# Optimization experiments

Hardware: AMD Instinct MI355X
Metric: run time of the kernel (lower is better)

Reference implementation:

```python
import jax, jax.numpy as jnp
import numpy as np

HIDDEN = 32  # hard-coded in EdgeModel's Sequential

def setup_inputs() -> dict:
    key = jax.random.key(0)
    ks = jax.random.split(key, 9)
    E, FN, FE, OUT = 200000, 512, 256, 128
    IN = FN + FN + FE  # 1280
    src = jax.random.normal(ks[0], (E, FN), dtype=jnp.float32)
    dest = jax.random.normal(ks[1], (E, FN), dtype=jnp.float32)
    edge_attr = jax.random.normal(ks[2], (E, FE), dtype=jnp.float32)
    u = jax.random.normal(ks[3], (64, 128), dtype=jnp.float32)
    batch = jax.random.randint(ks[4], (E,), 0, 64, dtype=jnp.int64)
    # Linear params, PyTorch default init scale ~ 1/sqrt(fan_in)
    s1 = 1.0 / np.sqrt(IN)
    s2 = 1.0 / np.sqrt(HIDDEN)
    W1 = jax.random.uniform(ks[5], (IN, HIDDEN), jnp.float32, -s1, s1)
    b1 = jax.random.uniform(ks[6], (HIDDEN,), jnp.float32, -s1, s1)
    W2 = jax.random.uniform(ks[7], (HIDDEN, OUT), jnp.float32, -s2, s2)
    b2 = jax.random.uniform(ks[8], (OUT,), jnp.float32, -s2, s2)
    return {"src": src, "dest": dest, "edge_attr": edge_attr, "u": u,
            "batch": batch, "W1": W1, "b1": b1, "W2": W2, "b2": b2}

def reference(src, dest, edge_attr, u, batch, W1, b1, W2, b2):
    # concat along feature dim, then Linear -> ELU -> Linear (u, batch unused)
    x = jnp.concatenate([src, dest, edge_attr], axis=1)  # [E, 2*FN+FE]
    h = jax.nn.elu(x @ W1 + b1)                           # [E, 32]
    return h @ W2 + b2                                    # [E, OUT]
```

## Files before the change

### kernel.cpp

```cpp
#include <hip/hip_runtime.h>
#include <hip/hip_bf16.h>

typedef __bf16 bf16x8 __attribute__((ext_vector_type(8)));
typedef unsigned short u16x8 __attribute__((ext_vector_type(8)));
typedef float f32x4 __attribute__((ext_vector_type(4)));
typedef unsigned int u32x4 __attribute__((ext_vector_type(4)));

using gptr_t = const __attribute__((address_space(1))) unsigned int*;
using lptr_t = __attribute__((address_space(3))) unsigned int*;

__global__ __launch_bounds__(256) void prep_w_kernel(
    const float* __restrict__ W1, const float* __restrict__ W2,
    unsigned short* __restrict__ wsB1, unsigned short* __restrict__ wsB2) {
  int tid = blockIdx.x * 256 + threadIdx.x;
  if (tid < 40960) {
    int j = tid & 7, l = (tid >> 3) & 63, nt = (tid >> 9) & 1, kt = tid >> 10;
    int k = kt * 32 + ((l >> 4) << 3) + j;
    int n = nt * 16 + (l & 15);
    __bf16 v = (__bf16)W1[k * 32 + n];
    wsB1[tid] = __builtin_bit_cast(unsigned short, v);
  } else if (tid < 45056) {
    int t = tid - 40960;
    int j = t & 7, l = (t >> 3) & 63, nt = t >> 9;
    int k = ((l >> 4) << 3) + j;
    int n = nt * 16 + (l & 15);
    __bf16 v = (__bf16)W2[k * 128 + n];
    wsB2[t] = __builtin_bit_cast(unsigned short, v);
  }
}

__device__ __forceinline__ u32x4 make_srd(const void* p, unsigned bytes) {
  u32x4 r;
  r[0] = (unsigned)(unsigned long long)p;
  r[1] = (unsigned)(((unsigned long long)p) >> 32);
  r[2] = bytes;
  r[3] = 0x00020000u;
  return r;
}

#define XLDS(SLOT, GP, FOFF)                                                   \
  do {                                                                         \
    __builtin_amdgcn_global_load_lds((gptr_t)(const void*)((GP) + (FOFF)),     \
                                     (lptr_t)(void*)(ringw + (SLOT) * 512),    \
                                     16, 0, 0);                                \
    __builtin_amdgcn_global_load_lds((gptr_t)(const void*)((GP) + (FOFF) + 4), \
                                     (lptr_t)(void*)(ringw + (SLOT) * 512 + 256), \
                                     16, 0, 0);                                \
  } while (0)
#define WLD(SLOT, SOFF)                                                    \
  asm volatile("buffer_load_dwordx4 %0, %2, %3, %4 offen offset:0"         \
               "\n\tbuffer_load_dwordx4 %1, %2, %3, %4 offen offset:1024"  \
               : "=&v"(pw[SLOT][0]), "=&v"(pw[SLOT][1])                    \
               : "v"(voffw), "s"(srdw), "s"((unsigned)(SOFF))              \
               : "memory")
#define VMW(N)                                                \
  do {                                                        \
    asm volatile("s_waitcnt vmcnt(" #N ")" ::: "memory");     \
    __builtin_amdgcn_sched_barrier(0);                        \
  } while (0)
#define CONS(SX, SW)                                                          \
  do {                                                                        \
    f32x4 lo, hi;                                                             \
    asm volatile("ds_read_b128 %0, %2\n\t"                                    \
                 "ds_read_b128 %1, %2 offset:1024\n\t"                        \
                 "s_waitcnt lgkmcnt(0)"                                       \
                 : "=&v"(lo), "=&v"(hi)                                       \
                 : "v"(ldsrd + (SX) * 2048u)                                  \
                 : "memory");                                                 \
    __builtin_amdgcn_sched_barrier(0);                                        \
    bf16x8 a;                                                                 \
    a[0] = (__bf16)lo[0]; a[1] = (__bf16)lo[1];                               \
    a[2] = (__bf16)lo[2]; a[3] = (__bf16)lo[3];                               \
    a[4] = (__bf16)hi[0]; a[5] = (__bf16)hi[1];                               \
    a[6] = (__bf16)hi[2]; a[7] = (__bf16)hi[3];                               \
    acc0 = __builtin_amdgcn_mfma_f32_16x16x32_bf16(                           \
        a, __builtin_bit_cast(bf16x8, pw[SW][0]), acc0, 0, 0, 0);             \
    acc1 = __builtin_amdgcn_mfma_f32_16x16x32_bf16(                           \
        a, __builtin_bit_cast(bf16x8, pw[SW][1]), acc1, 0, 0, 0);             \
  } while (0)

template <bool USE_WS>
__global__ __launch_bounds__(256, 3) void edge_mlp_kernel(
    const float* __restrict__ src, const float* __restrict__ dst,
    const float* __restrict__ ea, const float* __restrict__ W1,
    const float* __restrict__ b1, const float* __restrict__ W2,
    const float* __restrict__ b2, const unsigned short* __restrict__ wsB1,
    const unsigned short* __restrict__ wsB2, float* __restrict__ out, int nE) {
  __shared__ alignas(16) float ring_s[4][6][512];
  const int lane = threadIdx.x & 63;
  const int wave = threadIdx.x >> 6;
  const int l15 = lane & 15;
  const int lh = lane >> 4;
  const long strip = (long)blockIdx.x * 4 + wave;
  const long e0 = strip * 16;
  if (e0 >= nE) return;
  long row = e0 + l15;
  if (row >= nE) row = nE - 1;

  float* ringw = &ring_s[wave][0][0];
  const float bias0 = b1[l15];
  const float bias1 = b1[16 + l15];

  f32x4 acc0 = {0.f, 0.f, 0.f, 0.f};
  f32x4 acc1 = {0.f, 0.f, 0.f, 0.f};

  if constexpr (USE_WS) {
    const u32x4 srdw = make_srd(wsB1, 81920u);
    const unsigned voffw = (unsigned)lane * 16u;
    const float* psrc = src + row * 512 + lh * 8;
    const float* pdst = dst + row * 512 + lh * 8;
    const float* pea = ea + row * 256 + lh * 8;
    const unsigned ldsrd =
        (unsigned)(unsigned long long)(__attribute__((address_space(3))) void*)
            ringw + (unsigned)lane * 16u;

    u16x8 pw[4][2];

    XLDS(0, psrc, 0);    WLD(0, 0);
    XLDS(1, psrc, 32);   WLD(1, 2048);
    XLDS(2, psrc, 64);   WLD(2, 4096);
    XLDS(3, psrc, 96);   WLD(3, 6144);
    XLDS(4, psrc, 128);
    XLDS(5, psrc, 160);

    VMW(16); CONS(0, 0); XLDS(0, psrc, 192); WLD(0, 8192);
    VMW(16); CONS(1, 1); XLDS(1, psrc, 224); WLD(1, 10240);
    VMW(16); CONS(2, 2); XLDS(2, psrc, 256); WLD(2, 12288);
    VMW(16); CONS(3, 3); XLDS(3, psrc, 288); WLD(3, 14336);
    VMW(12); CONS(4, 0); XLDS(4, psrc, 320); WLD(0, 16384);
    VMW(12); CONS(5, 1); XLDS(5, psrc, 352); WLD(1, 18432);
    VMW(12); CONS(0, 2); XLDS(0, psrc, 384); WLD(2, 20480);
    VMW(12); CONS(1, 3); XLDS(1, psrc, 416); WLD(3, 22528);
    VMW(12); CONS(2, 0); XLDS(2, psrc, 448); WLD(0, 24576);
    VMW(12); CONS(3, 1); XLDS(3, psrc, 480); WLD(1, 26624);
    VMW(12); CONS(4, 2); XLDS(4, pdst, 0);   WLD(2, 28672);
    VMW(12); CONS(5, 3); XLDS(5, pdst, 32);  WLD(3, 30720);
    VMW(12); CONS(0, 0); XLDS(0, pdst, 64);  WLD(0, 32768);
    VMW(12); CONS(1, 1); XLDS(1, pdst, 96);  WLD(1, 34816);
    VMW(12); CONS(2, 2); XLDS(2, pdst, 128); WLD(2, 36864);
    VMW(12); CONS(3, 3); XLDS(3, pdst, 160); WLD(3, 38912);
    VMW(12); CONS(4, 0); XLDS(4, pdst, 192); WLD(0, 40960);
    VMW(12); CONS(5, 1); XLDS(5, pdst, 224); WLD(1, 43008);
    VMW(12); CONS(0, 2); XLDS(0, pdst, 256); WLD(2, 45056);
    VMW(12); CONS(1, 3); XLDS(1, pdst, 288); WLD(3, 47104);
    VMW(12); CONS(2, 0); XLDS(2, pdst, 320); WLD(0, 49152);
    VMW(12); CONS(3, 1); XLDS(3, pdst, 352); WLD(1, 51200);
    VMW(12); CONS(4, 2); XLDS(4, pdst, 384); WLD(2, 53248);
    VMW(12); CONS(5, 3); XLDS(5, pdst, 416); WLD(3, 55296);
    VMW(12); CONS(0, 0); XLDS(0, pdst, 448); WLD(0, 57344);
    VMW(12); CONS(1, 1); XLDS(1, pdst, 480); WLD(1, 59392);
    VMW(12); CONS(2, 2); XLDS(2, pea, 0);    WLD(2, 61440);
    VMW(12); CONS(3, 3); XLDS(3, pea, 32);   WLD(3, 63488);
    VMW(12); CONS(4, 0); XLDS(4, pea, 64);   WLD(0, 65536);
    VMW(12); CONS(5, 1); XLDS(5, pea, 96);   WLD(1, 67584);
    VMW(12); CONS(0, 2); XLDS(0, pea, 128);  WLD(2, 69632);
    VMW(12); CONS(1, 3); XLDS(1, pea, 160);  WLD(3, 71680);
    VMW(12); CONS(2, 0); XLDS(2, pea, 192);  WLD(0, 73728);
    VMW(12); CONS(3, 1); XLDS(3, pea, 224);  WLD(1, 75776);
    VMW(12); CONS(4, 2);                     WLD(2, 77824);
    VMW(10); CONS(5, 3);                     WLD(3, 79872);
    VMW(8);  CONS(0, 0);
    VMW(4);  CONS(1, 1);
    VMW(2);  CONS(2, 2);
    VMW(0);  CONS(3, 3);
  } else {
    for (int t = 0; t < 40; ++t) {
      const float* p = (t < 16) ? (src + row * 512 + t * 32 + lh * 8)
                     : (t < 32) ? (dst + row * 512 + (t - 16) * 32 + lh * 8)
                                : (ea + row * 256 + (t - 32) * 32 + lh * 8);
      f32x4 lo = *(const f32x4*)p;
      f32x4 hi = *(const f32x4*)(p + 4);
      bf16x8 a, bf0, bf1;
      a[0] = (__bf16)lo[0]; a[1] = (__bf16)lo[1];
      a[2] = (__bf16)lo[2]; a[3] = (__bf16)lo[3];
      a[4] = (__bf16)hi[0]; a[5] = (__bf16)hi[1];
      a[6] = (__bf16)hi[2]; a[7] = (__bf16)hi[3];
#pragma unroll
      for (int j = 0; j < 8; ++j) {
        int k = t * 32 + lh * 8 + j;
        bf0[j] = (__bf16)W1[k * 32 + l15];
        bf1[j] = (__bf16)W1[k * 32 + 16 + l15];
      }
      acc0 = __builtin_amdgcn_mfma_f32_16x16x32_bf16(a, bf0, acc0, 0, 0, 0);
      acc1 = __builtin_amdgcn_mfma_f32_16x16x32_bf16(a, bf1, acc1, 0, 0, 0);
    }
  }

  unsigned short* hl = (unsigned short*)ringw;
#pragma unroll
  for (int r = 0; r < 4; ++r) {
    int hrow = lh * 4 + r;
    float h0 = acc0[r] + bias0;
    float h1 = acc1[r] + bias1;
    h0 = h0 > 0.f ? h0 : (__expf(h0) - 1.f);
    h1 = h1 > 0.f ? h1 : (__expf(h1) - 1.f);
    __bf16 v0 = (__bf16)h0, v1 = (__bf16)h1;
    hl[hrow * 40 + l15] = __builtin_bit_cast(unsigned short, v0);
    hl[hrow * 40 + 16 + l15] = __builtin_bit_cast(unsigned short, v1);
  }
  asm volatile("s_waitcnt lgkmcnt(0)" ::: "memory");
  __builtin_amdgcn_sched_barrier(0);
  bf16x8 ha =
      __builtin_bit_cast(bf16x8, *(const u16x8*)(hl + l15 * 40 + lh * 8));

  f32x4 o[8];
#pragma unroll
  for (int nt = 0; nt < 8; ++nt) {
    bf16x8 bw;
    if (USE_WS) {
      bw = __builtin_bit_cast(bf16x8, *(const u16x8*)(wsB2 + nt * 512 + lane * 8));
    } else {
#pragma unroll
      for (int j = 0; j < 8; ++j)
        bw[j] = (__bf16)W2[(lh * 8 + j) * 128 + nt * 16 + l15];
    }
    f32x4 z = {0.f, 0.f, 0.f, 0.f};
    o[nt] = __builtin_amdgcn_mfma_f32_16x16x32_bf16(ha, bw, z, 0, 0, 0);
  }

#pragma unroll
  for (int nt = 0; nt < 8; ++nt) {
    float bb = b2[nt * 16 + l15];
#pragma unroll
    for (int r = 0; r < 4; ++r) {
      long e = e0 + lh * 4 + r;
      if (e < nE) out[e * 128 + nt * 16 + l15] = o[nt][r] + bb;
    }
  }
}

extern "C" void kernel_launch(void* const* d_in, const int* in_sizes, int n_in,
                              void* d_out, int out_size, void* d_ws,
                              size_t ws_size, hipStream_t stream) {
  const float* src = (const float*)d_in[0];
  const float* dst = (const float*)d_in[1];
  const float* ea = (const float*)d_in[2];
  const float* W1 = (const float*)d_in[5];
  const float* b1 = (const float*)d_in[6];
  const float* W2 = (const float*)d_in[7];
  const float* b2 = (const float*)d_in[8];
  float* out = (float*)d_out;

  const int nE = in_sizes[0] / 512;
  const long strips = (nE + 15) / 16;
  const int nblocks = (int)((strips + 3) / 4);

  unsigned short* wsB1 = (unsigned short*)d_ws;
  unsigned short* wsB2 = wsB1 + 40960;
  const bool use_ws = ws_size >= 45056 * sizeof(unsigned short);

  if (use_ws) {
    prep_w_kernel<<<176, 256, 0, stream>>>(W1, W2, wsB1, wsB2);
    edge_mlp_kernel<true><<<nblocks, 256, 0, stream>>>(
        src, dst, ea, W1, b1, W2, b2, wsB1, wsB2, out, nE);
  } else {
    edge_mlp_kernel<false><<<nblocks, 256, 0, stream>>>(
        src, dst, ea, W1, b1, W2, b2, nullptr, nullptr, out, nE);
  }
}
```

Measured before the change: 252.4 us.

## Load row-contiguous 64-float chunks into swizzled LDS ring for coalesced reads

Changes the global-to-LDS load pattern so each wave loads 16 consecutive floats per row (4 rows per instruction, 64 floats per row per stage) instead of 8-float fragments per row, with an XOR swizzle on both the store and ds_read addresses to avoid bank conflicts. The ring becomes 3 slots of 64-K chunks, and each stage consumes two MFMA k-steps, with 6 weight register sets in flight. The goal is better coalescing and fewer, larger pipeline stages. The fast path now requires nE divisible by 16 because the row clamp was removed.

```diff
diff --git a/kernel.cpp b/kernel.cpp
--- a/kernel.cpp
+++ b/kernel.cpp
@@ -8,6 +8,8 @@
 
 using gptr_t = const __attribute__((address_space(1))) unsigned int*;
 using lptr_t = __attribute__((address_space(3))) unsigned int*;
+#define gp(x) ((gptr_t)(const void*)(x))
+#define lp(x) ((lptr_t)(void*)(x))
 
 __global__ __launch_bounds__(256) void prep_w_kernel(
     const float* __restrict__ W1, const float* __restrict__ W2,
@@ -38,14 +40,16 @@
   return r;
 }
 
-#define XLDS(SLOT, GP, FOFF)                                                   \
+#define XST(SLOT, P, FOFF, RSTR)                                               \
   do {                                                                         \
-    __builtin_amdgcn_global_load_lds((gptr_t)(const void*)((GP) + (FOFF)),     \
-                                     (lptr_t)(void*)(ringw + (SLOT) * 512),    \
-                                     16, 0, 0);                                \
-    __builtin_amdgcn_global_load_lds((gptr_t)(const void*)((GP) + (FOFF) + 4), \
-                                     (lptr_t)(void*)(ringw + (SLOT) * 512 + 256), \
-                                     16, 0, 0);                                \
+    __builtin_amdgcn_global_load_lds(gp((P) + (FOFF)),                         \
+                                     lp(ringw + (SLOT) * 1024), 16, 0, 0);     \
+    __builtin_amdgcn_global_load_lds(gp((P) + (FOFF) + 4 * (RSTR)),            \
+                                     lp(ringw + (SLOT) * 1024 + 256), 16, 0, 0); \
+    __builtin_amdgcn_global_load_lds(gp((P) + (FOFF) + 8 * (RSTR)),            \
+                                     lp(ringw + (SLOT) * 1024 + 512), 16, 0, 0); \
+    __builtin_amdgcn_global_load_lds(gp((P) + (FOFF) + 12 * (RSTR)),           \
+                                     lp(ringw + (SLOT) * 1024 + 768), 16, 0, 0); \
   } while (0)
 #define WLD(SLOT, SOFF)                                                    \
   asm volatile("buffer_load_dwordx4 %0, %2, %3, %4 offen offset:0"         \
@@ -58,14 +62,15 @@
     asm volatile("s_waitcnt vmcnt(" #N ")" ::: "memory");     \
     __builtin_amdgcn_sched_barrier(0);                        \
   } while (0)
-#define CONS(SX, SW)                                                          \
+#define CONS(T)                                                               \
   do {                                                                        \
     f32x4 lo, hi;                                                             \
     asm volatile("ds_read_b128 %0, %2\n\t"                                    \
-                 "ds_read_b128 %1, %2 offset:1024\n\t"                        \
+                 "ds_read_b128 %1, %2 offset:16\n\t"                          \
                  "s_waitcnt lgkmcnt(0)"                                       \
                  : "=&v"(lo), "=&v"(hi)                                       \
-                 : "v"(ldsrd + (SX) * 2048u)                                  \
+                 : "v"(ldsrd + (unsigned)((((T) >> 1) % 3) * 4096 +           \
+                                          ((T)&1) * 128))                     \
                  : "memory");                                                 \
     __builtin_amdgcn_sched_barrier(0);                                        \
     bf16x8 a;                                                                 \
@@ -74,9 +79,9 @@
     a[4] = (__bf16)hi[0]; a[5] = (__bf16)hi[1];                               \
     a[6] = (__bf16)hi[2]; a[7] = (__bf16)hi[3];                               \
     acc0 = __builtin_amdgcn_mfma_f32_16x16x32_bf16(                           \
-        a, __builtin_bit_cast(bf16x8, pw[SW][0]), acc0, 0, 0, 0);             \
+        a, __builtin_bit_cast(bf16x8, pw[(T) % 6][0]), acc0, 0, 0, 0);        \
     acc1 = __builtin_amdgcn_mfma_f32_16x16x32_bf16(                           \
-        a, __builtin_bit_cast(bf16x8, pw[SW][1]), acc1, 0, 0, 0);             \
+        a, __builtin_bit_cast(bf16x8, pw[(T) % 6][1]), acc1, 0, 0, 0);        \
   } while (0)
 
 template <bool USE_WS>
@@ -86,7 +91,7 @@
     const float* __restrict__ b1, const float* __restrict__ W2,
     const float* __restrict__ b2, const unsigned short* __restrict__ wsB1,
     const unsigned short* __restrict__ wsB2, float* __restrict__ out, int nE) {
-  __shared__ alignas(16) float ring_s[4][6][512];
+  __shared__ alignas(16) float ring_s[4][3][1024];
   const int lane = threadIdx.x & 63;
   const int wave = threadIdx.x >> 6;
   const int l15 = lane & 15;
@@ -94,8 +99,6 @@
   const long strip = (long)blockIdx.x * 4 + wave;
   const long e0 = strip * 16;
   if (e0 >= nE) return;
-  long row = e0 + l15;
-  if (row >= nE) row = nE - 1;
 
   float* ringw = &ring_s[wave][0][0];
   const float bias0 = b1[l15];
@@ -107,67 +110,47 @@
   if constexpr (USE_WS) {
     const u32x4 srdw = make_srd(wsB1, 81920u);
     const unsigned voffw = (unsigned)lane * 16u;
-    const float* psrc = src + row * 512 + lh * 8;
-    const float* pdst = dst + row * 512 + lh * 8;
-    const float* pea = ea + row * 256 + lh * 8;
+    const unsigned xoffF = ((unsigned)l15 * 4u) ^ ((unsigned)lh * 8u);
+    const float* pSL = src + (size_t)(e0 + lh) * 512 + xoffF;
+    const float* pDL = dst + (size_t)(e0 + lh) * 512 + xoffF;
+    const float* pEL = ea + (size_t)(e0 + lh) * 256 + xoffF;
+    const unsigned rdswz = (unsigned)l15 * 256u +
+                           (((unsigned)lh * 32u) ^ ((unsigned)(l15 & 3) << 5));
     const unsigned ldsrd =
         (unsigned)(unsigned long long)(__attribute__((address_space(3))) void*)
-            ringw + (unsigned)lane * 16u;
-
-    u16x8 pw[4][2];
-
-    XLDS(0, psrc, 0);    WLD(0, 0);
-    XLDS(1, psrc, 32);   WLD(1, 2048);
-    XLDS(2, psrc, 64);   WLD(2, 4096);
-    XLDS(3, psrc, 96);   WLD(3, 6144);
-    XLDS(4, psrc, 128);
-    XLDS(5, psrc, 160);
-
-    VMW(16); CONS(0, 0); XLDS(0, psrc, 192); WLD(0, 8192);
-    VMW(16); CONS(1, 1); XLDS(1, psrc, 224); WLD(1, 10240);
-    VMW(16); CONS(2, 2); XLDS(2, psrc, 256); WLD(2, 12288);
-    VMW(16); CONS(3, 3); XLDS(3, psrc, 288); WLD(3, 14336);
-    VMW(12); CONS(4, 0); XLDS(4, psrc, 320); WLD(0, 16384);
-    VMW(12); CONS(5, 1); XLDS(5, psrc, 352); WLD(1, 18432);
-    VMW(12); CONS(0, 2); XLDS(0, psrc, 384); WLD(2, 20480);
-    VMW(12); CONS(1, 3); XLDS(1, psrc, 416); WLD(3, 22528);
-    VMW(12); CONS(2, 0); XLDS(2, psrc, 448); WLD(0, 24576);
-    VMW(12); CONS(3, 1); XLDS(3, psrc, 480); WLD(1, 26624);
-    VMW(12); CONS(4, 2); XLDS(4, pdst, 0);   WLD(2, 28672);
-    VMW(12); CONS(5, 3); XLDS(5, pdst, 32);  WLD(3, 30720);
-    VMW(12); CONS(0, 0); XLDS(0, pdst, 64);  WLD(0, 32768);
-    VMW(12); CONS(1, 1); XLDS(1, pdst, 96);  WLD(1, 34816);
-    VMW(12); CONS(2, 2); XLDS(2, pdst, 128); WLD(2, 36864);
-    VMW(12); CONS(3, 3); XLDS(3, pdst, 160); WLD(3, 38912);
-    VMW(12); CONS(4, 0); XLDS(4, pdst, 192); WLD(0, 40960);
-    VMW(12); CONS(5, 1); XLDS(5, pdst, 224); WLD(1, 43008);
-    VMW(12); CONS(0, 2); XLDS(0, pdst, 256); WLD(2, 45056);
-    VMW(12); CONS(1, 3); XLDS(1, pdst, 288); WLD(3, 47104);
-    VMW(12); CONS(2, 0); XLDS(2, pdst, 320); WLD(0, 49152);
-    VMW(12); CONS(3, 1); XLDS(3, pdst, 352); WLD(1, 51200);
-    VMW(12); CONS(4, 2); XLDS(4, pdst, 384); WLD(2, 53248);
-    VMW(12); CONS(5, 3); XLDS(5, pdst, 416); WLD(3, 55296);
-    VMW(12); CONS(0, 0); XLDS(0, pdst, 448); WLD(0, 57344);
-    VMW(12); CONS(1, 1); XLDS(1, pdst, 480); WLD(1, 59392);
-    VMW(12); CONS(2, 2); XLDS(2, pea, 0);    WLD(2, 61440);
-    VMW(12); CONS(3, 3); XLDS(3, pea, 32);   WLD(3, 63488);
-    VMW(12); CONS(4, 0); XLDS(4, pea, 64);   WLD(0, 65536);
-    VMW(12); CONS(5, 1); XLDS(5, pea, 96);   WLD(1, 67584);
-    VMW(12); CONS(0, 2); XLDS(0, pea, 128);  WLD(2, 69632);
-    VMW(12); CONS(1, 3); XLDS(1, pea, 160);  WLD(3, 71680);
-    VMW(12); CONS(2, 0); XLDS(2, pea, 192);  WLD(0, 73728);
-    VMW(12); CONS(3, 1); XLDS(3, pea, 224);  WLD(1, 75776);
-    VMW(12); CONS(4, 2);                     WLD(2, 77824);
-    VMW(10); CONS(5, 3);                     WLD(3, 79872);
-    VMW(8);  CONS(0, 0);
-    VMW(4);  CONS(1, 1);
-    VMW(2);  CONS(2, 2);
-    VMW(0);  CONS(3, 3);
+            ringw + rdswz;
+
+    u16x8 pw[6][2];
+
+    XST(0, pSL, 0, 512);  WLD(0, 0);    WLD(1, 2048);
+    XST(1, pSL, 64, 512); WLD(2, 4096); WLD(3, 6144);
+    VMW(6); CONS(0);  CONS(1);  XST(2, pSL, 128, 512); WLD(4, 8192);  WLD(5, 10240);
+    VMW(6); CONS(2);  CONS(3);  XST(0, pSL, 192, 512); WLD(0, 12288); WLD(1, 14336);
+    VMW(6); CONS(4);  CONS(5);  XST(1, pSL, 256, 512); WLD(2, 16384); WLD(3, 18432);
+    VMW(6); CONS(6);  CONS(7);  XST(2, pSL, 320, 512); WLD(4, 20480); WLD(5, 22528);
+    VMW(6); CONS(8);  CONS(9);  XST(0, pSL, 384, 512); WLD(0, 24576); WLD(1, 26624);
+    VMW(6); CONS(10); CONS(11); XST(1, pSL, 448, 512); WLD(2, 28672); WLD(3, 30720);
+    VMW(6); CONS(12); CONS(13); XST(2, pDL, 0, 512);   WLD(4, 32768); WLD(5, 34816);
+    VMW(6); CONS(14); CONS(15); XST(0, pDL, 64, 512);  WLD(0, 36864); WLD(1, 38912);
+    VMW(6); CONS(16); CONS(17); XST(1, pDL, 128, 512); WLD(2, 40960); WLD(3, 43008);
+    VMW(6); CONS(18); CONS(19); XST(2, pDL, 192, 512); WLD(4, 45056); WLD(5, 47104);
+    VMW(6); CONS(20); CONS(21); XST(0, pDL, 256, 512); WLD(0, 49152); WLD(1, 51200);
+    VMW(6); CONS(22); CONS(23); XST(1, pDL, 320, 512); WLD(2, 53248); WLD(3, 55296);
+    VMW(6); CONS(24); CONS(25); XST(2, pDL, 384, 512); WLD(4, 57344); WLD(5, 59392);
+    VMW(6); CONS(26); CONS(27); XST(0, pDL, 448, 512); WLD(0, 61440); WLD(1, 63488);
+    VMW(6); CONS(28); CONS(29); XST(1, pEL, 0, 256);   WLD(2, 65536); WLD(3, 67584);
+    VMW(6); CONS(30); CONS(31); XST(2, pEL, 64, 256);  WLD(4, 69632); WLD(5, 71680);
+    VMW(6); CONS(32); CONS(33); XST(0, pEL, 128, 256); WLD(0, 73728); WLD(1, 75776);
+    VMW(6); CONS(34); CONS(35); XST(1, pEL, 192, 256); WLD(2, 77824); WLD(3, 79872);
+    VMW(6); CONS(36); CONS(37);
+    VMW(0); CONS(38); CONS(39);
   } else {
+    long rowf = e0 + l15;
+    if (rowf >= nE) rowf = nE - 1;
     for (int t = 0; t < 40; ++t) {
-      const float* p = (t < 16) ? (src + row * 512 + t * 32 + lh * 8)
-                     : (t < 32) ? (dst + row * 512 + (t - 16) * 32 + lh * 8)
-                                : (ea + row * 256 + (t - 32) * 32 + lh * 8);
+      const float* p = (t < 16) ? (src + rowf * 512 + t * 32 + lh * 8)
+                     : (t < 32) ? (dst + rowf * 512 + (t - 16) * 32 + lh * 8)
+                                : (ea + rowf * 256 + (t - 32) * 32 + lh * 8);
       f32x4 lo = *(const f32x4*)p;
       f32x4 hi = *(const f32x4*)(p + 4);
       bf16x8 a, bf0, bf1;
@@ -247,7 +230,8 @@
 
   unsigned short* wsB1 = (unsigned short*)d_ws;
   unsigned short* wsB2 = wsB1 + 40960;
-  const bool use_ws = ws_size >= 45056 * sizeof(unsigned short);
+  const bool use_ws =
+      ws_size >= 45056 * sizeof(unsigned short) && (nE & 15) == 0;
 
   if (use_ws) {
     prep_w_kernel<<<176, 256, 0, stream>>>(W1, W2, wsB1, wsB2);
```

Result: faster. 246.8 us (-2.2%).
